# Performance work log

Hardware: AMD Instinct MI355X
Metric: run time of the kernel (lower is better)

Reference implementation:

```python
import jax, jax.numpy as jnp
import numpy as np

N = 50000      # nodes
E = 500000     # edges (avg degree 10)
G = 64         # graphs (events)
IN = 7
H = 64
EPS = 1e-5


def setup_inputs() -> dict:
    key = jax.random.key(0)
    ks = iter(jax.random.split(key, 64))
    d = {}
    d["x"] = jax.random.normal(next(ks), (N, IN), jnp.float32)
    d["edge_index"] = jax.random.randint(next(ks), (2, E), 0, N, dtype=jnp.int32)
    d["batch"] = jnp.sort(jax.random.randint(next(ks), (N,), 0, G, dtype=jnp.int32))
    dims = [(IN, H), (H, 2 * H), (2 * H, 4 * H)]
    for i, (ic, oc) in enumerate(dims, 1):
        d[f"b{i}_W1"] = jax.random.normal(next(ks), (2 * ic, oc), jnp.float32) * 0.05
        d[f"b{i}_b1"] = jnp.zeros((oc,), jnp.float32)
        d[f"b{i}_g1"] = jnp.ones((oc,), jnp.float32)
        d[f"b{i}_beta1"] = jnp.zeros((oc,), jnp.float32)
        d[f"b{i}_W2"] = jax.random.normal(next(ks), (oc, oc), jnp.float32) * 0.05
        d[f"b{i}_b2"] = jnp.zeros((oc,), jnp.float32)
        d[f"b{i}_g2"] = jnp.ones((oc,), jnp.float32)
        d[f"b{i}_beta2"] = jnp.zeros((oc,), jnp.float32)
    d["head_W1"] = jax.random.normal(next(ks), (4 * H, 2 * H), jnp.float32) * 0.05
    d["head_b1"] = jnp.zeros((2 * H,), jnp.float32)
    d["head_W2"] = jax.random.normal(next(ks), (2 * H, 2), jnp.float32) * 0.05
    d["head_b2"] = jnp.zeros((2,), jnp.float32)
    return d


def _bn(h, g, b):
    # BatchNorm1d in training mode: batch statistics over edge dim
    m = h.mean(axis=0)
    v = h.var(axis=0)
    return (h - m) * jax.lax.rsqrt(v + EPS) * g + b


def _edgeconv(x, src, dst, W1, b1, g1, be1, W2, b2, g2, be2):
    # PyG EdgeConv: message = MLP(cat[x_i, x_j - x_i]), aggregated at target i=dst
    xi = x[dst]                                   # [E, C]
    xj = x[src]                                   # [E, C]
    e = jnp.concatenate([xi, xj - xi], axis=-1)   # [E, 2C]
    h = jax.nn.relu(_bn(e @ W1 + b1, g1, be1))
    h = jax.nn.relu(_bn(h @ W2 + b2, g2, be2))
    s = jax.ops.segment_sum(h, dst, num_segments=N)
    cnt = jax.ops.segment_sum(jnp.ones((h.shape[0],), h.dtype), dst, num_segments=N)
    return s / jnp.maximum(cnt, 1.0)[:, None]     # mean aggregation


def reference(x, edge_index, batch,
              b1_W1, b1_b1, b1_g1, b1_beta1, b1_W2, b1_b2, b1_g2, b1_beta2,
              b2_W1, b2_b1, b2_g1, b2_beta1, b2_W2, b2_b2, b2_g2, b2_beta2,
              b3_W1, b3_b1, b3_g1, b3_beta1, b3_W2, b3_b2, b3_g2, b3_beta2,
              head_W1, head_b1, head_W2, head_b2):
    src, dst = edge_index[0], edge_index[1]
    h = _edgeconv(x, src, dst, b1_W1, b1_b1, b1_g1, b1_beta1, b1_W2, b1_b2, b1_g2, b1_beta2)
    h = _edgeconv(h, src, dst, b2_W1, b2_b1, b2_g1, b2_beta1, b2_W2, b2_b2, b2_g2, b2_beta2)
    h = _edgeconv(h, src, dst, b3_W1, b3_b1, b3_g1, b3_beta1, b3_W2, b3_b2, b3_g2, b3_beta2)
    # global mean pool per graph
    s = jax.ops.segment_sum(h, batch, num_segments=G)
    cnt = jax.ops.segment_sum(jnp.ones((N,), h.dtype), batch, num_segments=G)
    g = s / jnp.maximum(cnt, 1.0)[:, None]        # [G, 256]
    # head (dropout is identity in eval)
    z = jax.nn.relu(g @ head_W1 + head_b1)
    return z @ head_W2 + head_b2                  # [G, 2]
```

## Files before the change

### kernel.cpp

```cpp
#include <hip/hip_runtime.h>
#include <stdint.h>

constexpr int NN = 50000;
constexpr int NE = 500000;
constexpr int NG = 64;
constexpr float BN_EPS = 1e-5f;

typedef __attribute__((ext_vector_type(8))) short bf16x8;
typedef __attribute__((ext_vector_type(4))) float f32x4;

__device__ inline float bf2f(unsigned short u) {
    return __uint_as_float(((unsigned int)u) << 16);
}
__device__ inline float bf2f_lo(unsigned int u) {
    return __uint_as_float((u & 0xffffu) << 16);
}
__device__ inline float bf2f_hi(unsigned int u) {
    return __uint_as_float(u & 0xffff0000u);
}
__device__ inline unsigned short f2bf_rne(float f) {
    unsigned int u = __float_as_uint(f);
    unsigned int r = (u + 0x7fffu + ((u >> 16) & 1u)) >> 16;
    return (unsigned short)r;
}

template<int CPT> __device__ inline void load_row(const float* p, float* o) {
    if constexpr (CPT == 2) { float2 v = *(const float2*)p; o[0]=v.x; o[1]=v.y; }
    else if constexpr (CPT == 4) { float4 v = *(const float4*)p; o[0]=v.x; o[1]=v.y; o[2]=v.z; o[3]=v.w; }
    else { load_row<4>(p, o); load_row<4>(p+4, o+4); }
}
template<int CPT> __device__ inline void store_row(float* p, const float* v) {
    if constexpr (CPT == 2) { *(float2*)p = make_float2(v[0], v[1]); }
    else if constexpr (CPT == 4) { *(float4*)p = make_float4(v[0], v[1], v[2], v[3]); }
    else { store_row<4>(p, v); store_row<4>(p+4, v+4); }
}
template<int CPT> __device__ inline void store_hi(unsigned short* p, const float* v) {
    unsigned int w[CPT / 2];
    #pragma unroll
    for (int j = 0; j < CPT / 2; j++)
        w[j] = (unsigned int)f2bf_rne(v[2*j]) | ((unsigned int)f2bf_rne(v[2*j+1]) << 16);
    if constexpr (CPT == 2) { *(unsigned int*)p = w[0]; }
    else if constexpr (CPT == 4) { *(uint2*)p = uint2{w[0], w[1]}; }
    else { *(uint4*)p = uint4{w[0], w[1], w[2], w[3]}; }
}
__device__ inline void unpack8(uint4 u, float* f) {
    f[0]=bf2f_lo(u.x); f[1]=bf2f_hi(u.x);
    f[2]=bf2f_lo(u.y); f[3]=bf2f_hi(u.y);
    f[4]=bf2f_lo(u.z); f[5]=bf2f_hi(u.z);
    f[6]=bf2f_lo(u.w); f[7]=bf2f_hi(u.w);
}

__global__ void k_zero16(uint4* p, int n) {
    int i = blockIdx.x * 256 + threadIdx.x;
    if (i < n) p[i] = uint4{0u, 0u, 0u, 0u};
}

__global__ void k_diag(float* out, int n, float val) {
    int i = blockIdx.x * 256 + threadIdx.x;
    if (i < n) out[i] = val;
}

__global__ void k_deg(const int* __restrict__ idx, int* __restrict__ cnt) {
    int e = blockIdx.x * 256 + threadIdx.x;
    if (e < NE) atomicAdd(&cnt[idx[e]], 1);
}

__global__ void k_scan(const int* __restrict__ degi, int* __restrict__ rowptr) {
    __shared__ int buf[1024];
    __shared__ int carry_s;
    const int tid = threadIdx.x;
    if (tid == 0) carry_s = 0;
    __syncthreads();
    for (int base = 0; base < NN; base += 1024) {
        int i = base + tid;
        int v = (i < NN) ? degi[i] : 0;
        buf[tid] = v;
        __syncthreads();
        for (int off = 1; off < 1024; off <<= 1) {
            int t = (tid >= off) ? buf[tid - off] : 0;
            __syncthreads();
            buf[tid] += t;
            __syncthreads();
        }
        if (i < NN) rowptr[i] = carry_s + buf[tid] - v;
        __syncthreads();
        if (tid == 0) carry_s += buf[1023];
        __syncthreads();
    }
    if (tid == 0) rowptr[NN] = carry_s;
}

__global__ void k_fill(const int* __restrict__ dst, const int* __restrict__ rowptr,
                       int* __restrict__ cursor, int* __restrict__ eidx) {
    int e = blockIdx.x * 256 + threadIdx.x;
    if (e < NE) {
        int d = dst[e];
        int p = atomicAdd(&cursor[d], 1);
        eidx[rowptr[d] + p] = e;
    }
}

__global__ void k_grange(const int* __restrict__ batch, int* __restrict__ gse) {
    int n = blockIdx.x * 256 + threadIdx.x;
    if (n >= NN) return;
    int b = batch[n];
    if (n == 0 || batch[n-1] != b) gse[b] = n;
    if (n == NN-1 || batch[n+1] != b) gse[NG + b] = n + 1;
}

template<int OC>
__global__ void k_bnfin(const float* __restrict__ st, const float* __restrict__ g,
                        const float* __restrict__ be, float* __restrict__ dv) {
    int c = threadIdx.x;
    const float invE = 1.0f / (float)NE;
    float m = st[c] * invE;
    float v = st[OC + c] * invE - m * m;
    float sc = g[c] * rsqrtf(v + BN_EPS);
    dv[c] = sc;
    dv[OC + c] = be[c] - m * sc;
}

template<int OC>
__global__ void k_packW(const float* __restrict__ W,
                        unsigned short* __restrict__ Wph, unsigned short* __restrict__ Wpl) {
    constexpr int NT = OC / 16;
    const int l = threadIdx.x;
    const int ktnt = blockIdx.x;
    const int n = (ktnt % NT) * 16 + (l & 15);
    const int kbase = (ktnt / NT) * 32 + (l >> 4) * 8;
    size_t fo = ((size_t)ktnt * 64 + l) * 8;
    #pragma unroll
    for (int b = 0; b < 8; b++) {
        float w = W[(size_t)(kbase + b) * OC + n];
        unsigned short h = f2bf_rne(w);
        Wph[fo + b] = h;
        Wpl[fo + b] = f2bf_rne(w - bf2f(h));
    }
}

template<int CIN, int OC>
__global__ __launch_bounds__(256) void k_nodeproj(
    const float* __restrict__ x, const float* __restrict__ W1,
    const float* __restrict__ b1, float* __restrict__ A, float* __restrict__ Bn,
    unsigned short* __restrict__ Ah, unsigned short* __restrict__ Bh)
{
    constexpr int SP = CIN + 1;
    constexpr int CPT = OC / 32;
    __shared__ float xs[32 * SP];
    const int t = threadIdx.x;
    const int n0 = blockIdx.x * 32;
    {
        const int el = t >> 3, l8 = t & 7;
        int n = n0 + el; if (n >= NN) n = NN - 1;
        const float* xp = x + (size_t)n * CIN;
        for (int k = l8; k < CIN; k += 8) xs[el * SP + k] = xp[k];
    }
    __syncthreads();
    const int tx = t & 31, ty = t >> 5;
    float accA[4][CPT], accB[4][CPT];
    #pragma unroll
    for (int i = 0; i < 4; i++)
        #pragma unroll
        for (int j = 0; j < CPT; j++) { accA[i][j] = 0.f; accB[i][j] = 0.f; }

    const float* Wa = W1 + tx * CPT;
    const float* Wb = W1 + (size_t)CIN * OC + tx * CPT;
    for (int k = 0; k < CIN; k++) {
        float wa[CPT], wb[CPT];
        load_row<CPT>(Wa + (size_t)k * OC, wa);
        load_row<CPT>(Wb + (size_t)k * OC, wb);
        #pragma unroll
        for (int i = 0; i < 4; i++) {
            float ev = xs[(ty * 4 + i) * SP + k];
            #pragma unroll
            for (int j = 0; j < CPT; j++) {
                accA[i][j] = fmaf(ev, wa[j] - wb[j], accA[i][j]);
                accB[i][j] = fmaf(ev, wb[j], accB[i][j]);
            }
        }
    }
    float bs[CPT];
    load_row<CPT>(b1 + tx * CPT, bs);
    #pragma unroll
    for (int i = 0; i < 4; i++) {
        const int n = n0 + ty * 4 + i;
        if (n < NN) {
            float va[CPT];
            #pragma unroll
            for (int j = 0; j < CPT; j++) va[j] = accA[i][j] + bs[j];
            store_row<CPT>(A  + (size_t)n * OC + tx * CPT, va);
            store_row<CPT>(Bn + (size_t)n * OC + tx * CPT, accB[i]);
            store_hi<CPT>(Ah + (size_t)n * OC + tx * CPT, va);
            store_hi<CPT>(Bh + (size_t)n * OC + tx * CPT, accB[i]);
        }
    }
}

template<int OC>
__global__ __launch_bounds__(512) void k_sgather(
    const float* __restrict__ Bn,
    const int* __restrict__ src, const int* __restrict__ dst,
    const int* __restrict__ eidx, float* __restrict__ S)
{
    constexpr int ETL = 128;
    constexpr int NSEG = 512 / OC;
    constexpr int RSEG = ETL / NSEG;
    __shared__ int sdst_s[ETL], ssrc_s[ETL];
    const int t = threadIdx.x;
    const int e0 = blockIdx.x * ETL;
    const int valid = (NE - e0 < ETL) ? (NE - e0) : ETL;
    if (t < ETL) {
        int dn = -1, sn = 0;
        if (t < valid) { int e = eidx[e0 + t]; dn = dst[e]; sn = src[e]; }
        sdst_s[t] = dn; ssrc_s[t] = sn;
    }
    __syncthreads();
    const int col = t % OC;
    const int rbeg = (t / OC) * RSEG;
    float a = 0.f; int cur = -1;
    for (int r = 0; r < RSEG; r++) {
        const int gr = rbeg + r;
        if (gr >= valid) break;
        const int nd = sdst_s[gr];
        float v = Bn[(size_t)ssrc_s[gr] * OC + col];
        if (nd != cur) {
            if (cur >= 0) atomicAdd(&S[(size_t)cur * OC + col], a);
            cur = nd; a = 0.f;
        }
        a += v;
    }
    if (cur >= 0) atomicAdd(&S[(size_t)cur * OC + col], a);
}

template<int OC>
__global__ __launch_bounds__(256) void k_snode(
    const float* __restrict__ A, const float* __restrict__ Bn,
    const float* __restrict__ S,
    const int* __restrict__ degi, const int* __restrict__ dego,
    float* __restrict__ stats)
{
    constexpr int CPT = OC / 32;
    __shared__ float reds[4 * OC];
    __shared__ float redq[4 * OC];
    const int t = threadIdx.x;
    const int l32 = t & 31, grp = t >> 5;
    float s[CPT], q[CPT];
    #pragma unroll
    for (int j = 0; j < CPT; j++) { s[j] = 0.f; q[j] = 0.f; }
    for (int n = blockIdx.x * 8 + grp; n < NN; n += 8192) {
        const float dI = (float)degi[n], dO = (float)dego[n];
        float av[CPT], bv[CPT], sv[CPT];
        load_row<CPT>(A  + (size_t)n * OC + l32 * CPT, av);
        load_row<CPT>(Bn + (size_t)n * OC + l32 * CPT, bv);
        load_row<CPT>(S  + (size_t)n * OC + l32 * CPT, sv);
        #pragma unroll
        for (int j = 0; j < CPT; j++) {
            s[j] += dI * av[j] + dO * bv[j];
            q[j] += dI * av[j] * av[j] + dO * bv[j] * bv[j] + 2.f * av[j] * sv[j];
        }
    }
    #pragma unroll
    for (int j = 0; j < CPT; j++) {
        s[j] += __shfl_down(s[j], 32);
        q[j] += __shfl_down(q[j], 32);
    }
    const int w = t >> 6, lane = t & 63;
    if (lane < 32) {
        #pragma unroll
        for (int j = 0; j < CPT; j++) {
            reds[w * OC + lane * CPT + j] = s[j];
            redq[w * OC + lane * CPT + j] = q[j];
        }
    }
    __syncthreads();
    for (int c = t; c < OC; c += 256) {
        float S2 = reds[c] + reds[OC + c] + reds[2 * OC + c] + reds[3 * OC + c];
        float Q2 = redq[c] + redq[OC + c] + redq[2 * OC + c] + redq[3 * OC + c];
        atomicAdd(&stats[c], S2);
        atomicAdd(&stats[OC + c], Q2);
    }
}

template<int OC, int MODE>
__global__ __launch_bounds__(512, 3) void k_efuse(
    const float* __restrict__ A, const float* __restrict__ Bn,
    const unsigned short* __restrict__ Ah, const unsigned short* __restrict__ Bh,
    const int* __restrict__ src, const int* __restrict__ dst,
    const int* __restrict__ eidx,
    const unsigned short* __restrict__ Wph, const unsigned short* __restrict__ Wpl,
    const float* __restrict__ b2,
    const float* __restrict__ dv1, float* __restrict__ stats,
    const float* __restrict__ dv2, float* __restrict__ xout)
{
    constexpr int ETL = 128;
    constexpr int NT = OC / 16;
    constexpr int NTW = NT / 4;
    constexpr int NCH = OC / 64;
    constexpr int SROWS = 8192 / OC;
    constexpr int NSTRIP = ETL / SROWS;
    constexpr int YSTR = OC + 4;
    constexpr int YB = SROWS * YSTR * 4;
    constexpr int TB = (MODE == 0) ? 16384 : 32768;
    constexpr int SMB = (MODE == 1 && YB > TB) ? YB : TB;
    constexpr int NSEG = 512 / OC;
    constexpr int RSEG = SROWS / NSEG;

    __shared__ __align__(16) unsigned char smem[SMB];
    __shared__ int sdst_s[ETL], ssrc_s[ETL];

    const int t = threadIdx.x;
    const int e0 = blockIdx.x * ETL;
    const int valid = (NE - e0 < ETL) ? (NE - e0) : ETL;

    if (t < ETL) {
        int dn = -1, sn = 0;
        if (t < valid) { int e = eidx[e0 + t]; dn = dst[e]; sn = src[e]; }
        sdst_s[t] = dn; ssrc_s[t] = sn;
    }
    __syncthreads();

    const int lane = t & 63, wave = t >> 6;
    const int rg = wave >> 2, ch = wave & 3;
    const int lr = lane & 15, lg = lane >> 4;

    f32x4 acc[4][NTW];
    #pragma unroll
    for (int m = 0; m < 4; m++)
        #pragma unroll
        for (int n = 0; n < NTW; n++) acc[m][n] = (f32x4){0.f, 0.f, 0.f, 0.f};

    const int brow = t >> 2, q = t & 3;
    const bool rvalid = (brow < valid);

    for (int kc = 0; kc < NCH; kc++) {
        {
            const int gc0 = kc * 64 + q * 16;
            if (rvalid) {
                float af[16], bfv[16];
                if constexpr (MODE == 0) {
                    const unsigned short* Ar = Ah + (size_t)sdst_s[brow] * OC + gc0;
                    const unsigned short* Br = Bh + (size_t)ssrc_s[brow] * OC + gc0;
                    unpack8(*(const uint4*)(Ar), af);
                    unpack8(*(const uint4*)(Ar + 8), af + 8);
                    unpack8(*(const uint4*)(Br), bfv);
                    unpack8(*(const uint4*)(Br + 8), bfv + 8);
                } else {
                    const float* Ar = A  + (size_t)sdst_s[brow] * OC + gc0;
                    const float* Br = Bn + (size_t)ssrc_s[brow] * OC + gc0;
                    load_row<8>(Ar, af);     load_row<8>(Ar + 8, af + 8);
                    load_row<8>(Br, bfv);    load_row<8>(Br + 8, bfv + 8);
                }
                #pragma unroll
                for (int i = 0; i < 4; i++) {
                    float4 sc = *(const float4*)(dv1 + gc0 + i * 4);
                    float4 sh = *(const float4*)(dv1 + OC + gc0 + i * 4);
                    float tv[4];
                    tv[0] = fmaxf(fmaf(af[i*4+0] + bfv[i*4+0], sc.x, sh.x), 0.f);
                    tv[1] = fmaxf(fmaf(af[i*4+1] + bfv[i*4+1], sc.y, sh.y), 0.f);
                    tv[2] = fmaxf(fmaf(af[i*4+2] + bfv[i*4+2], sc.z, sh.z), 0.f);
                    tv[3] = fmaxf(fmaf(af[i*4+3] + bfv[i*4+3], sc.w, sh.w), 0.f);
                    unsigned short hv[4];
                    #pragma unroll
                    for (int j = 0; j < 4; j++) hv[j] = f2bf_rne(tv[j]);
                    const int byt = (brow * 128 + q * 32 + i * 8) ^ ((brow & 7) << 4);
                    *(ushort4*)(smem + byt) = *(ushort4*)hv;
                    if constexpr (MODE == 1) {
                        unsigned short lv[4];
                        #pragma unroll
                        for (int j = 0; j < 4; j++) lv[j] = f2bf_rne(tv[j] - bf2f(hv[j]));
                        *(ushort4*)(smem + 16384 + byt) = *(ushort4*)lv;
                    }
                }
            } else {
                const ushort4 z = ushort4{0, 0, 0, 0};
                #pragma unroll
                for (int i = 0; i < 4; i++) {
                    const int byt = (brow * 128 + q * 32 + i * 8) ^ ((brow & 7) << 4);
                    *(ushort4*)(smem + byt) = z;
                    if constexpr (MODE == 1) *(ushort4*)(smem + 16384 + byt) = z;
                }
            }
        }
        __syncthreads();

        #pragma unroll
        for (int kt2 = 0; kt2 < 2; kt2++) {
            bf16x8 ah[4], al[4];
            #pragma unroll
            for (int m = 0; m < 4; m++) {
                const int r = rg * 64 + m * 16 + lr;
                const int byt = (r * 128 + kt2 * 64 + lg * 16) ^ ((r & 7) << 4);
                ah[m] = *(const bf16x8*)(smem + byt);
                if constexpr (MODE == 1) al[m] = *(const bf16x8*)(smem + 16384 + byt);
            }
            #pragma unroll
            for (int n = 0; n < NTW; n++) {
                const size_t fo = ((size_t)((kc * 2 + kt2) * NT + ch * NTW + n) * 64 + lane) * 8;
                bf16x8 wh = *(const bf16x8*)(Wph + fo);
                if constexpr (MODE == 0) {
                    #pragma unroll
                    for (int m = 0; m < 4; m++)
                        acc[m][n] = __builtin_amdgcn_mfma_f32_16x16x32_bf16(ah[m], wh, acc[m][n], 0, 0, 0);
                } else {
                    bf16x8 wl = *(const bf16x8*)(Wpl + fo);
                    #pragma unroll
                    for (int m = 0; m < 4; m++) {
                        acc[m][n] = __builtin_amdgcn_mfma_f32_16x16x32_bf16(ah[m], wh, acc[m][n], 0, 0, 0);
                        acc[m][n] = __builtin_amdgcn_mfma_f32_16x16x32_bf16(ah[m], wl, acc[m][n], 0, 0, 0);
                        acc[m][n] = __builtin_amdgcn_mfma_f32_16x16x32_bf16(al[m], wh, acc[m][n], 0, 0, 0);
                    }
                }
            }
        }
        __syncthreads();
    }

    if constexpr (MODE == 0) {
        #pragma unroll
        for (int n = 0; n < NTW; n++) {
            const int col = (ch * NTW + n) * 16 + lr;
            const float bb = b2[col];
            float s = 0.f, qq = 0.f;
            #pragma unroll
            for (int m = 0; m < 4; m++) {
                const int rbase = rg * 64 + m * 16 + lg * 4;
                #pragma unroll
                for (int e = 0; e < 4; e++) {
                    float h = (rbase + e < valid) ? (acc[m][n][e] + bb) : 0.f;
                    s += h; qq += h * h;
                }
            }
            s += __shfl_xor(s, 16); s += __shfl_xor(s, 32);
            qq += __shfl_xor(qq, 16); qq += __shfl_xor(qq, 32);
            if (lg == 0) {
                atomicAdd(&stats[col], s);
                atomicAdd(&stats[OC + col], qq);
            }
        }
    } else {
        float* yt = (float*)smem;
        const int acol = t % OC;
        const int aseg = t / OC;
        #pragma unroll
        for (int s = 0; s < NSTRIP; s++) {
            const int r0 = s * SROWS;
            #pragma unroll
            for (int m = 0; m < 4; m++) {
                const int base = rg * 64 + m * 16;
                if (base >= r0 && base < r0 + SROWS) {
                    #pragma unroll
                    for (int n = 0; n < NTW; n++) {
                        const int col = (ch * NTW + n) * 16 + lr;
                        const float bb = b2[col], scv = dv2[col], shv = dv2[OC + col];
                        #pragma unroll
                        for (int e = 0; e < 4; e++) {
                            const int rl = base - r0 + lg * 4 + e;
                            yt[rl * YSTR + col] = fmaxf(fmaf(acc[m][n][e] + bb, scv, shv), 0.f);
                        }
                    }
                }
            }
            __syncthreads();
            {
                const int rbeg = aseg * RSEG;
                float a = 0.f; int cur = -1;
                for (int r = 0; r < RSEG; r++) {
                    const int gr = r0 + rbeg + r;
                    if (gr >= valid) break;
                    const int nd = sdst_s[gr];
                    if (nd != cur) {
                        if (cur >= 0) atomicAdd(&xout[(size_t)cur * OC + acol], a);
                        cur = nd; a = 0.f;
                    }
                    a += yt[(rbeg + r) * YSTR + acol];
                }
                if (cur >= 0) atomicAdd(&xout[(size_t)cur * OC + acol], a);
            }
            __syncthreads();
        }
    }
}

template<int OC>
__global__ __launch_bounds__(256) void k_div(float* __restrict__ xout,
                                             const int* __restrict__ degi) {
    constexpr int CPT = OC / 32;
    const int tx = threadIdx.x & 31;
    const int n = blockIdx.x * 8 + (threadIdx.x >> 5);
    if (n >= NN) return;
    const float inv = 1.0f / fmaxf((float)degi[n], 1.0f);
    float v[CPT];
    load_row<CPT>(xout + (size_t)n * OC + tx * CPT, v);
    #pragma unroll
    for (int j = 0; j < CPT; j++) v[j] *= inv;
    store_row<CPT>(xout + (size_t)n * OC + tx * CPT, v);
}

__global__ void k_pool(const float* __restrict__ x3, const int* __restrict__ gse,
                       float* __restrict__ pooled) {
    const int g = blockIdx.x, c = threadIdx.x;
    const int beg = gse[g], end = gse[NG + g];
    float s = 0.f;
    for (int n = beg; n < end; n++) s += x3[(size_t)n * 256 + c];
    pooled[g * 256 + c] = s / fmaxf((float)(end - beg), 1.0f);
}

__global__ void k_head(const float* __restrict__ pooled,
                       const float* __restrict__ W1, const float* __restrict__ b1,
                       const float* __restrict__ W2, const float* __restrict__ b2,
                       float* __restrict__ out) {
    __shared__ float gv[256];
    __shared__ float z[128];
    const int g = blockIdx.x;
    gv[threadIdx.x] = pooled[g * 256 + threadIdx.x];
    __syncthreads();
    if (threadIdx.x < 128) {
        const int c = threadIdx.x;
        float s = b1[c];
        for (int k = 0; k < 256; k++) s = fmaf(gv[k], W1[k * 128 + c], s);
        z[c] = fmaxf(s, 0.f);
    }
    __syncthreads();
    if (threadIdx.x < 2) {
        const int o = threadIdx.x;
        float s = b2[o];
        for (int k = 0; k < 128; k++) s = fmaf(z[k], W2[k * 2 + o], s);
        out[g * 2 + o] = s;
    }
}

template<int CIN, int OC>
static void run_block(const float* xin, const float* const* Q,
                      float* A, float* B, unsigned short* Ah, unsigned short* Bh,
                      const int* src, const int* dst,
                      const int* eidx, const unsigned short* Wph, const unsigned short* Wpl,
                      float* st, float* dv, const int* degi, const int* dego,
                      float* xout, hipStream_t s)
{
    const int EG = (NE + 127) / 128;
    float* S = xout;
    k_nodeproj<CIN, OC><<<(NN + 31) / 32, 256, 0, s>>>(xin, Q[0], Q[1], A, B, Ah, Bh);
    k_zero16<<<((NN * OC / 4) + 255) / 256, 256, 0, s>>>((uint4*)S, NN * OC / 4);
    k_sgather<OC><<<EG, 512, 0, s>>>(B, src, dst, eidx, S);
    k_snode<OC><<<1024, 256, 0, s>>>(A, B, S, degi, dego, st);
    k_bnfin<OC><<<1, OC, 0, s>>>(st, Q[2], Q[3], dv);
    k_efuse<OC, 0><<<EG, 512, 0, s>>>(A, B, Ah, Bh, src, dst, eidx, Wph, Wpl, Q[5], dv, st + 512, nullptr, nullptr);
    k_bnfin<OC><<<1, OC, 0, s>>>(st + 512, Q[6], Q[7], dv + 512);
    k_zero16<<<((NN * OC / 4) + 255) / 256, 256, 0, s>>>((uint4*)xout, NN * OC / 4);
    k_efuse<OC, 1><<<EG, 512, 0, s>>>(A, B, Ah, Bh, src, dst, eidx, Wph, Wpl, Q[5], dv, nullptr, dv + 512, xout);
    k_div<OC><<<(NN + 7) / 8, 256, 0, s>>>(xout, degi);
}

extern "C" void kernel_launch(void* const* d_in, const int* in_sizes, int n_in,
                              void* d_out, int out_size, void* d_ws, size_t ws_size,
                              hipStream_t stream)
{
    (void)in_sizes; (void)n_in;
    const float* x = (const float*)d_in[0];
    const int* ei = (const int*)d_in[1];
    const int* src = ei;
    const int* dst = ei + NE;
    const int* batch = (const int*)d_in[2];
    const float* P[28];
    for (int i = 0; i < 28; i++) P[i] = (const float*)d_in[3 + i];
    float* out = (float*)d_out;

    size_t offs[21];
    {
        size_t o = 0;
        auto take = [&](size_t bytes) -> size_t {
            size_t r = o; o = (o + bytes + 255) & ~(size_t)255; return r;
        };
        offs[0] = take((size_t)NN * 256 * 4);
        offs[1] = take((size_t)NN * 256 * 4);
        offs[2] = take((size_t)NN * 256 * 4);
        offs[3] = take((size_t)NN * 128 * 4);
        offs[4] = o;
        offs[5] = take((size_t)NN * 4);
        offs[6] = take((size_t)NN * 4);
        offs[7] = take((size_t)NN * 4);
        offs[8] = take(3 * 1024 * 4);
        offs[9] = take(2 * NG * 4);
        offs[10] = o;
        offs[11] = take((size_t)(NN + 1) * 4);
        offs[12] = take((size_t)NE * 4);
        offs[13] = take(3 * 1024 * 4);
        offs[14] = take((size_t)NG * 256 * 4);
        offs[15] = take((64*64 + 128*128 + 256*256) * 2);
        offs[16] = take((64*64 + 128*128 + 256*256) * 2);
        offs[17] = take((size_t)NN * 256 * 2);
        offs[18] = take((size_t)NN * 256 * 2);
        offs[19] = o;
        if (ws_size < o) {
            float val = 1000.0f + (float)(ws_size >> 20);
            k_diag<<<(out_size + 255) / 256, 256, 0, stream>>>(out, out_size, val);
            return;
        }
    }

    char* W = (char*)d_ws;
    float* A  = (float*)(W + offs[0]);
    float* B  = (float*)(W + offs[1]);
    float* xa = (float*)(W + offs[2]);
    float* xb = (float*)(W + offs[3]);
    int* degi = (int*)(W + offs[5]);
    int* dego = (int*)(W + offs[6]);
    int* cursor = (int*)(W + offs[7]);
    float* stats = (float*)(W + offs[8]);
    int* gse = (int*)(W + offs[9]);
    int* rowptr = (int*)(W + offs[11]);
    int* eidx = (int*)(W + offs[12]);
    float* dv = (float*)(W + offs[13]);
    float* pooled = (float*)(W + offs[14]);
    unsigned short* Wph = (unsigned short*)(W + offs[15]);
    unsigned short* Wpl = (unsigned short*)(W + offs[16]);
    unsigned short* Ah = (unsigned short*)(W + offs[17]);
    unsigned short* Bh = (unsigned short*)(W + offs[18]);
    unsigned short* Wph1 = Wph,            * Wpl1 = Wpl;
    unsigned short* Wph2 = Wph + 64*64,    * Wpl2 = Wpl + 64*64;
    unsigned short* Wph3 = Wph2 + 128*128, * Wpl3 = Wpl2 + 128*128;

    int nz = (int)((offs[10] - offs[4]) / 16);
    k_zero16<<<(nz + 255) / 256, 256, 0, stream>>>((uint4*)(W + offs[4]), nz);

    k_deg<<<(NE + 255) / 256, 256, 0, stream>>>(dst, degi);
    k_deg<<<(NE + 255) / 256, 256, 0, stream>>>(src, dego);
    k_scan<<<1, 1024, 0, stream>>>(degi, rowptr);
    k_fill<<<(NE + 255) / 256, 256, 0, stream>>>(dst, rowptr, cursor, eidx);
    k_grange<<<(NN + 255) / 256, 256, 0, stream>>>(batch, gse);

    k_packW<64> <<<(64/32)*(64/16),   64, 0, stream>>>(P[4],  Wph1, Wpl1);
    k_packW<128><<<(128/32)*(128/16), 64, 0, stream>>>(P[12], Wph2, Wpl2);
    k_packW<256><<<(256/32)*(256/16), 64, 0, stream>>>(P[20], Wph3, Wpl3);

    run_block<7,   64>(x,  P + 0,  A, B, Ah, Bh, src, dst, eidx, Wph1, Wpl1, stats + 0,    dv + 0,    degi, dego, xa, stream);
    run_block<64, 128>(xa, P + 8,  A, B, Ah, Bh, src, dst, eidx, Wph2, Wpl2, stats + 1024, dv + 1024, degi, dego, xb, stream);
    run_block<128,256>(xb, P + 16, A, B, Ah, Bh, src, dst, eidx, Wph3, Wpl3, stats + 2048, dv + 2048, degi, dego, xa, stream);

    k_pool<<<NG, 256, 0, stream>>>(xa, gse, pooled);
    k_head<<<NG, 256, 0, stream>>>(pooled, P[24], P[25], P[26], P[27], out);
}
```

Before: 2.617 ms.

## Drop fp32 node projections and use bf16 copies in stats, gather and second pass

Removes the fp32 A/B per-node projection buffers and makes k_sgather, k_snode and the MODE 1 k_efuse pass read the bf16 Ah/Bh copies instead. The gather now handles two columns per thread with 32-bit loads. The aim is to roughly halve the bytes written by nodeproj and read by the gather, stats and second edge passes. In exchange the BatchNorm statistics and outputs are computed from bf16-rounded projections, which costs accuracy.

New measurement: 2.458 ms. -6.1%, faster.

```diff
diff --git a/kernel.cpp b/kernel.cpp
--- a/kernel.cpp
+++ b/kernel.cpp
@@ -48,6 +48,17 @@
     f[2]=bf2f_lo(u.y); f[3]=bf2f_hi(u.y);
     f[4]=bf2f_lo(u.z); f[5]=bf2f_hi(u.z);
     f[6]=bf2f_lo(u.w); f[7]=bf2f_hi(u.w);
+}
+template<int CPT> __device__ inline void load_hi(const unsigned short* p, float* o) {
+    if constexpr (CPT == 2) {
+        unsigned int u = *(const unsigned int*)p;
+        o[0]=bf2f_lo(u); o[1]=bf2f_hi(u);
+    } else if constexpr (CPT == 4) {
+        uint2 u = *(const uint2*)p;
+        o[0]=bf2f_lo(u.x); o[1]=bf2f_hi(u.x); o[2]=bf2f_lo(u.y); o[3]=bf2f_hi(u.y);
+    } else {
+        unpack8(*(const uint4*)p, o);
+    }
 }
 
 __global__ void k_zero16(uint4* p, int n) {
@@ -141,7 +152,7 @@
 template<int CIN, int OC>
 __global__ __launch_bounds__(256) void k_nodeproj(
     const float* __restrict__ x, const float* __restrict__ W1,
-    const float* __restrict__ b1, float* __restrict__ A, float* __restrict__ Bn,
+    const float* __restrict__ b1,
     unsigned short* __restrict__ Ah, unsigned short* __restrict__ Bh)
 {
     constexpr int SP = CIN + 1;
@@ -188,8 +199,6 @@
             float va[CPT];
             #pragma unroll
             for (int j = 0; j < CPT; j++) va[j] = accA[i][j] + bs[j];
-            store_row<CPT>(A  + (size_t)n * OC + tx * CPT, va);
-            store_row<CPT>(Bn + (size_t)n * OC + tx * CPT, accB[i]);
             store_hi<CPT>(Ah + (size_t)n * OC + tx * CPT, va);
             store_hi<CPT>(Bh + (size_t)n * OC + tx * CPT, accB[i]);
         }
@@ -198,12 +207,13 @@
 
 template<int OC>
 __global__ __launch_bounds__(512) void k_sgather(
-    const float* __restrict__ Bn,
+    const unsigned short* __restrict__ Bh,
     const int* __restrict__ src, const int* __restrict__ dst,
     const int* __restrict__ eidx, float* __restrict__ S)
 {
     constexpr int ETL = 128;
-    constexpr int NSEG = 512 / OC;
+    constexpr int HC = OC / 2;
+    constexpr int NSEG = 512 / HC;
     constexpr int RSEG = ETL / NSEG;
     __shared__ int sdst_s[ETL], ssrc_s[ETL];
     const int t = threadIdx.x;
@@ -215,26 +225,32 @@
         sdst_s[t] = dn; ssrc_s[t] = sn;
     }
     __syncthreads();
-    const int col = t % OC;
-    const int rbeg = (t / OC) * RSEG;
-    float a = 0.f; int cur = -1;
+    const int cp = (t % HC) * 2;
+    const int rbeg = (t / HC) * RSEG;
+    float a0 = 0.f, a1 = 0.f; int cur = -1;
     for (int r = 0; r < RSEG; r++) {
         const int gr = rbeg + r;
         if (gr >= valid) break;
         const int nd = sdst_s[gr];
-        float v = Bn[(size_t)ssrc_s[gr] * OC + col];
+        unsigned int u = *(const unsigned int*)(Bh + (size_t)ssrc_s[gr] * OC + cp);
         if (nd != cur) {
-            if (cur >= 0) atomicAdd(&S[(size_t)cur * OC + col], a);
-            cur = nd; a = 0.f;
-        }
-        a += v;
-    }
-    if (cur >= 0) atomicAdd(&S[(size_t)cur * OC + col], a);
+            if (cur >= 0) {
+                atomicAdd(&S[(size_t)cur * OC + cp], a0);
+                atomicAdd(&S[(size_t)cur * OC + cp + 1], a1);
+            }
+            cur = nd; a0 = 0.f; a1 = 0.f;
+        }
+        a0 += bf2f_lo(u); a1 += bf2f_hi(u);
+    }
+    if (cur >= 0) {
+        atomicAdd(&S[(size_t)cur * OC + cp], a0);
+        atomicAdd(&S[(size_t)cur * OC + cp + 1], a1);
+    }
 }
 
 template<int OC>
 __global__ __launch_bounds__(256) void k_snode(
-    const float* __restrict__ A, const float* __restrict__ Bn,
+    const unsigned short* __restrict__ Ah, const unsigned short* __restrict__ Bh,
     const float* __restrict__ S,
     const int* __restrict__ degi, const int* __restrict__ dego,
     float* __restrict__ stats)
@@ -250,8 +266,8 @@
     for (int n = blockIdx.x * 8 + grp; n < NN; n += 8192) {
         const float dI = (float)degi[n], dO = (float)dego[n];
         float av[CPT], bv[CPT], sv[CPT];
-        load_row<CPT>(A  + (size_t)n * OC + l32 * CPT, av);
-        load_row<CPT>(Bn + (size_t)n * OC + l32 * CPT, bv);
+        load_hi<CPT>(Ah + (size_t)n * OC + l32 * CPT, av);
+        load_hi<CPT>(Bh + (size_t)n * OC + l32 * CPT, bv);
         load_row<CPT>(S  + (size_t)n * OC + l32 * CPT, sv);
         #pragma unroll
         for (int j = 0; j < CPT; j++) {
@@ -283,7 +299,6 @@
 
 template<int OC, int MODE>
 __global__ __launch_bounds__(512, 3) void k_efuse(
-    const float* __restrict__ A, const float* __restrict__ Bn,
     const unsigned short* __restrict__ Ah, const unsigned short* __restrict__ Bh,
     const int* __restrict__ src, const int* __restrict__ dst,
     const int* __restrict__ eidx,
@@ -337,19 +352,12 @@
             const int gc0 = kc * 64 + q * 16;
             if (rvalid) {
                 float af[16], bfv[16];
-                if constexpr (MODE == 0) {
-                    const unsigned short* Ar = Ah + (size_t)sdst_s[brow] * OC + gc0;
-                    const unsigned short* Br = Bh + (size_t)ssrc_s[brow] * OC + gc0;
-                    unpack8(*(const uint4*)(Ar), af);
-                    unpack8(*(const uint4*)(Ar + 8), af + 8);
-                    unpack8(*(const uint4*)(Br), bfv);
-                    unpack8(*(const uint4*)(Br + 8), bfv + 8);
-                } else {
-                    const float* Ar = A  + (size_t)sdst_s[brow] * OC + gc0;
-                    const float* Br = Bn + (size_t)ssrc_s[brow] * OC + gc0;
-                    load_row<8>(Ar, af);     load_row<8>(Ar + 8, af + 8);
-                    load_row<8>(Br, bfv);    load_row<8>(Br + 8, bfv + 8);
-                }
+                const unsigned short* Ar = Ah + (size_t)sdst_s[brow] * OC + gc0;
+                const unsigned short* Br = Bh + (size_t)ssrc_s[brow] * OC + gc0;
+                unpack8(*(const uint4*)(Ar), af);
+                unpack8(*(const uint4*)(Ar + 8), af + 8);
+                unpack8(*(const uint4*)(Br), bfv);
+                unpack8(*(const uint4*)(Br + 8), bfv + 8);
                 #pragma unroll
                 for (int i = 0; i < 4; i++) {
                     float4 sc = *(const float4*)(dv1 + gc0 + i * 4);
@@ -531,7 +539,7 @@
 
 template<int CIN, int OC>
 static void run_block(const float* xin, const float* const* Q,
-                      float* A, float* B, unsigned short* Ah, unsigned short* Bh,
+                      unsigned short* Ah, unsigned short* Bh,
                       const int* src, const int* dst,
                       const int* eidx, const unsigned short* Wph, const unsigned short* Wpl,
                       float* st, float* dv, const int* degi, const int* dego,
@@ -539,15 +547,15 @@
 {
     const int EG = (NE + 127) / 128;
     float* S = xout;
-    k_nodeproj<CIN, OC><<<(NN + 31) / 32, 256, 0, s>>>(xin, Q[0], Q[1], A, B, Ah, Bh);
+    k_nodeproj<CIN, OC><<<(NN + 31) / 32, 256, 0, s>>>(xin, Q[0], Q[1], Ah, Bh);
     k_zero16<<<((NN * OC / 4) + 255) / 256, 256, 0, s>>>((uint4*)S, NN * OC / 4);
-    k_sgather<OC><<<EG, 512, 0, s>>>(B, src, dst, eidx, S);
-    k_snode<OC><<<1024, 256, 0, s>>>(A, B, S, degi, dego, st);
+    k_sgather<OC><<<EG, 512, 0, s>>>(Bh, src, dst, eidx, S);
+    k_snode<OC><<<1024, 256, 0, s>>>(Ah, Bh, S, degi, dego, st);
     k_bnfin<OC><<<1, OC, 0, s>>>(st, Q[2], Q[3], dv);
-    k_efuse<OC, 0><<<EG, 512, 0, s>>>(A, B, Ah, Bh, src, dst, eidx, Wph, Wpl, Q[5], dv, st + 512, nullptr, nullptr);
+    k_efuse<OC, 0><<<EG, 512, 0, s>>>(Ah, Bh, src, dst, eidx, Wph, Wpl, Q[5], dv, st + 512, nullptr, nullptr);
     k_bnfin<OC><<<1, OC, 0, s>>>(st + 512, Q[6], Q[7], dv + 512);
     k_zero16<<<((NN * OC / 4) + 255) / 256, 256, 0, s>>>((uint4*)xout, NN * OC / 4);
-    k_efuse<OC, 1><<<EG, 512, 0, s>>>(A, B, Ah, Bh, src, dst, eidx, Wph, Wpl, Q[5], dv, nullptr, dv + 512, xout);
+    k_efuse<OC, 1><<<EG, 512, 0, s>>>(Ah, Bh, src, dst, eidx, Wph, Wpl, Q[5], dv, nullptr, dv + 512, xout);
     k_div<OC><<<(NN + 7) / 8, 256, 0, s>>>(xout, degi);
 }
 
@@ -565,14 +573,14 @@
     for (int i = 0; i < 28; i++) P[i] = (const float*)d_in[3 + i];
     float* out = (float*)d_out;
 
-    size_t offs[21];
+    size_t offs[19];
     {
         size_t o = 0;
         auto take = [&](size_t bytes) -> size_t {
             size_t r = o; o = (o + bytes + 255) & ~(size_t)255; return r;
         };
-        offs[0] = take((size_t)NN * 256 * 4);
-        offs[1] = take((size_t)NN * 256 * 4);
+        offs[0] = take((size_t)NN * 256 * 2);
+        offs[1] = take((size_t)NN * 256 * 2);
         offs[2] = take((size_t)NN * 256 * 4);
         offs[3] = take((size_t)NN * 128 * 4);
         offs[4] = o;
@@ -588,9 +596,7 @@
         offs[14] = take((size_t)NG * 256 * 4);
         offs[15] = take((64*64 + 128*128 + 256*256) * 2);
         offs[16] = take((64*64 + 128*128 + 256*256) * 2);
-        offs[17] = take((size_t)NN * 256 * 2);
-        offs[18] = take((size_t)NN * 256 * 2);
-        offs[19] = o;
+        offs[17] = o;
         if (ws_size < o) {
             float val = 1000.0f + (float)(ws_size >> 20);
             k_diag<<<(out_size + 255) / 256, 256, 0, stream>>>(out, out_size, val);
@@ -599,8 +605,8 @@
     }
 
     char* W = (char*)d_ws;
-    float* A  = (float*)(W + offs[0]);
-    float* B  = (float*)(W + offs[1]);
+    unsigned short* Ah = (unsigned short*)(W + offs[0]);
+    unsigned short* Bh = (unsigned short*)(W + offs[1]);
     float* xa = (float*)(W + offs[2]);
     float* xb = (float*)(W + offs[3]);
     int* degi = (int*)(W + offs[5]);
@@ -614,8 +620,6 @@
     float* pooled = (float*)(W + offs[14]);
     unsigned short* Wph = (unsigned short*)(W + offs[15]);
     unsigned short* Wpl = (unsigned short*)(W + offs[16]);
-    unsigned short* Ah = (unsigned short*)(W + offs[17]);
-    unsigned short* Bh = (unsigned short*)(W + offs[18]);
     unsigned short* Wph1 = Wph,            * Wpl1 = Wpl;
     unsigned short* Wph2 = Wph + 64*64,    * Wpl2 = Wpl + 64*64;
     unsigned short* Wph3 = Wph2 + 128*128, * Wpl3 = Wpl2 + 128*128;
@@ -633,9 +637,9 @@
     k_packW<128><<<(128/32)*(128/16), 64, 0, stream>>>(P[12], Wph2, Wpl2);
     k_packW<256><<<(256/32)*(256/16), 64, 0, stream>>>(P[20], Wph3, Wpl3);
 
-    run_block<7,   64>(x,  P + 0,  A, B, Ah, Bh, src, dst, eidx, Wph1, Wpl1, stats + 0,    dv + 0,    degi, dego, xa, stream);
-    run_block<64, 128>(xa, P + 8,  A, B, Ah, Bh, src, dst, eidx, Wph2, Wpl2, stats + 1024, dv + 1024, degi, dego, xb, stream);
-    run_block<128,256>(xb, P + 16, A, B, Ah, Bh, src, dst, eidx, Wph3, Wpl3, stats + 2048, dv + 2048, degi, dego, xa, stream);
+    run_block<7,   64>(x,  P + 0,  Ah, Bh, src, dst, eidx, Wph1, Wpl1, stats + 0,    dv + 0,    degi, dego, xa, stream);
+    run_block<64, 128>(xa, P + 8,  Ah, Bh, src, dst, eidx, Wph2, Wpl2, stats + 1024, dv + 1024, degi, dego, xb, stream);
+    run_block<128,256>(xb, P + 16, Ah, Bh, src, dst, eidx, Wph3, Wpl3, stats + 2048, dv + 2048, degi, dego, xa, stream);
 
     k_pool<<<NG, 256, 0, stream>>>(xa, gse, pooled);
     k_head<<<NG, 256, 0, stream>>>(pooled, P[24], P[25], P[26], P[27], out);
```
